# Kernel tuning notes

Measured on AMD Instinct MI355X. Metric: run time of the kernel, lower is better.

Reference implementation:

```python
import jax, jax.numpy as jnp
import numpy as np


def _structure_constants():
    # Octonion multiplication table: e_i * e_j = sum_k C[i,j,k] e_k.
    # e0 is the real unit; imaginary triples follow the standard Fano-plane
    # convention (Baez): e_a e_b = e_c for the cyclic triples below.
    C = np.zeros((8, 8, 8), dtype=np.float32)
    C[0, 0, 0] = 1.0
    for i in range(1, 8):
        C[0, i, i] = 1.0   # 1 * e_i = e_i
        C[i, 0, i] = 1.0   # e_i * 1 = e_i
        C[i, i, 0] = -1.0  # e_i * e_i = -1
    triples = [(1, 2, 3), (1, 4, 5), (1, 7, 6), (2, 4, 6), (2, 5, 7), (3, 4, 7), (3, 6, 5)]
    for (a, b, c) in triples:
        for (p, q, r) in ((a, b, c), (b, c, a), (c, a, b)):
            C[p, q, r] = 1.0
            C[q, p, r] = -1.0
    return C


_C = _structure_constants()

IN_FEATURES = 64
OUT_FEATURES = 64
BATCH = (16, 4096)


def setup_inputs() -> dict:
    key = jax.random.key(0)
    kx, kw, kb = jax.random.split(key, 3)
    x = jax.random.normal(kx, (*BATCH, IN_FEATURES, 8), dtype=jnp.float32)
    # 8 octonion-component weight matrices, stacked: [8, out, in]
    scale = 1.0 / np.sqrt(IN_FEATURES * 8)
    W = jax.random.normal(kw, (8, OUT_FEATURES, IN_FEATURES), dtype=jnp.float32) * scale
    b = jax.random.normal(kb, (OUT_FEATURES, 8), dtype=jnp.float32) * 0.01
    return {"x": x, "W": W, "b": b}


def reference(x, W, b):
    # out[..., o, k] = sum_{i,j,f} C[i,j,k] * W[i,o,f] * x[..., f, j] + b[o, k]
    # Fold the sparse structure constants into one block weight, then a single
    # contraction (the fused-GEMM formulation of the original 64-linear loop).
    C = jnp.asarray(_C, dtype=x.dtype)
    Wbig = jnp.einsum('iof,ijk->okfj', W, C)        # [out, 8, in, 8]
    out = jnp.einsum('...fj,okfj->...ok', x, Wbig)  # [..., out, 8]
    return out + b
```

## Files before the change

### kernel.cpp

```cpp
#include <hip/hip_runtime.h>
#include <hip/hip_bf16.h>

typedef __attribute__((ext_vector_type(8))) short short8;
typedef __attribute__((ext_vector_type(4))) float f32x4;
typedef __attribute__((address_space(1))) const unsigned int as1_u32;
typedef __attribute__((address_space(3))) unsigned int as3_u32;

#define BM 256
#define BN 256
#define BK 64
#define LDSTA 72
#define NKT 8
#define A_ELE (256 * LDSTA)
#define B_ELE (256 * 64)
#define LDS_BYTES ((2 * A_ELE + 2 * B_ELE) * 2)

static __device__ __forceinline__ unsigned short f2bf(float f) {
    union { __hip_bfloat16 h; unsigned short u; } cv;
    cv.h = __float2bfloat16(f);
    return cv.u;
}

__device__ __forceinline__ void gload16(const unsigned short* g, unsigned short* l) {
    __builtin_amdgcn_global_load_lds((as1_u32*)g, (as3_u32*)l, 16, 0, 0);
}

__global__ __launch_bounds__(256) void build_wbig(const float* __restrict__ W,
                                                  unsigned short* __restrict__ WbigS) {
    __shared__ float C[8][8][8];
    const int t = threadIdx.x;
    for (int i = t; i < 512; i += 256) ((float*)C)[i] = 0.0f;
    __syncthreads();
    if (t == 0) {
        C[0][0][0] = 1.0f;
        for (int i = 1; i < 8; ++i) { C[0][i][i] = 1.0f; C[i][0][i] = 1.0f; C[i][i][0] = -1.0f; }
        const int tr[7][3] = {{1,2,3},{1,4,5},{1,7,6},{2,4,6},{2,5,7},{3,4,7},{3,6,5}};
        for (int q = 0; q < 7; ++q) {
            const int a = tr[q][0], b = tr[q][1], c = tr[q][2];
            const int p[3][3] = {{a,b,c},{b,c,a},{c,a,b}};
            for (int u = 0; u < 3; ++u) {
                C[p[u][0]][p[u][1]][p[u][2]] = 1.0f;
                C[p[u][1]][p[u][0]][p[u][2]] = -1.0f;
            }
        }
    }
    __syncthreads();
    const int e = blockIdx.x * 256 + t;
    const int m = e >> 9, kk = e & 511;
    const int o = m >> 3, k = m & 7, f = kk >> 3, j = kk & 7;
    float s = 0.0f;
#pragma unroll
    for (int i = 0; i < 8; ++i) s += C[i][j][k] * W[i * 4096 + o * 64 + f];

    const int ntile = m >> 8, row = m & 255;
    const int kt = kk >> 6, c = kk & 63;
    const int g_st = (c >> 3) ^ (row & 7);
    WbigS[((((size_t)(ntile * 8 + kt) * 256 + row) * 8 + g_st) * 8) + (c & 7)] = f2bf(s);
}

__global__ __launch_bounds__(512, 2) void oct_gemm(const float* __restrict__ X,
                                                   const unsigned short* __restrict__ WbigS,
                                                   const float* __restrict__ Bias,
                                                   float* __restrict__ Out) {
    extern __shared__ unsigned short smem[];
    unsigned short* As[2] = { smem,             smem + A_ELE };
    unsigned short* Bs[2] = { smem + 2 * A_ELE, smem + 2 * A_ELE + B_ELE };

    const int bid   = blockIdx.x;
    const int xcd   = bid & 7;
    const int ix    = bid >> 3;
    const int mtile = xcd * 32 + (ix >> 1);
    const int ntile = ix & 1;
    const int rowBase = mtile * BM;
    const int colBase = ntile * BN;

    const int t    = threadIdx.x;
    const int lane = t & 63;
    const int w    = t >> 6;
    const int wr   = w >> 2;
    const int wc   = w & 3;
    const int l15  = lane & 15;
    const int l4   = lane >> 4;

    const int srow = t >> 3;
    const int scol = (t & 7) * 8;
    const float* Xrow = X + (size_t)(rowBase + srow) * 512 + scol;

    f32x4 va0[8], va1[8];

#define ISSUE_A(VA, KT) do { _Pragma("unroll") \
    for (int l = 0; l < 4; ++l) { \
        const float* src = Xrow + (size_t)(l * 64) * 512 + (KT) * BK; \
        VA[2*l]   = *reinterpret_cast<const f32x4*>(src); \
        VA[2*l+1] = *reinterpret_cast<const f32x4*>(src + 4); \
    } } while (0)

#define WRITE_A(VA, BUF) do { _Pragma("unroll") \
    for (int l = 0; l < 4; ++l) { \
        short8 p; \
        p[0]=(short)f2bf(VA[2*l][0]);   p[1]=(short)f2bf(VA[2*l][1]); \
        p[2]=(short)f2bf(VA[2*l][2]);   p[3]=(short)f2bf(VA[2*l][3]); \
        p[4]=(short)f2bf(VA[2*l+1][0]); p[5]=(short)f2bf(VA[2*l+1][1]); \
        p[6]=(short)f2bf(VA[2*l+1][2]); p[7]=(short)f2bf(VA[2*l+1][3]); \
        *reinterpret_cast<short8*>(&As[BUF][(l*64 + srow) * LDSTA + scol]) = p; \
    } } while (0)

#define GLOAD_B(BUF, KT) do { _Pragma("unroll") \
    for (int j = 0; j < 4; ++j) \
        gload16(WbigS + ((size_t)(ntile * 8 + (KT)) << 14) + (((w * 4 + j) * 64 + lane) << 3), \
                Bs[BUF] + ((w * 4 + j) << 9)); \
    } while (0)

    f32x4 acc[8][4];
#pragma unroll
    for (int ni = 0; ni < 4; ++ni) {
        const float bv = Bias[colBase + wc * 64 + ni * 16 + l15];
#pragma unroll
        for (int mi = 0; mi < 8; ++mi) acc[mi][ni] = (f32x4){bv, bv, bv, bv};
    }

    ISSUE_A(va0, 0);
    GLOAD_B(0, 0);
    ISSUE_A(va1, 1);
    WRITE_A(va0, 0);
    asm volatile("s_waitcnt vmcnt(8) lgkmcnt(0)" ::: "memory");
    __builtin_amdgcn_s_barrier();

#pragma unroll
    for (int kt = 0; kt < NKT; ++kt) {
        if (kt + 1 < NKT) GLOAD_B((kt + 1) & 1, kt + 1);
        if (kt + 2 < NKT) { if ((kt & 1) == 0) ISSUE_A(va0, kt + 2); else ISSUE_A(va1, kt + 2); }
        __builtin_amdgcn_sched_barrier(0);

#pragma unroll
        for (int kk = 0; kk < 2; ++kk) {
            short8 b[4];
#pragma unroll
            for (int ni = 0; ni < 4; ++ni) {
                const int row = wc * 64 + ni * 16 + l15;
                const int gs  = ((kk * 4 + l4) ^ (l15 & 7)) * 8;
                b[ni] = *reinterpret_cast<const short8*>(&Bs[kt & 1][row * 64 + gs]);
            }
            __builtin_amdgcn_s_setprio(1);
#pragma unroll
            for (int mi = 0; mi < 8; ++mi) {
                const short8 a = *reinterpret_cast<const short8*>(
                    &As[kt & 1][(wr * 128 + mi * 16 + l15) * LDSTA + kk * 32 + l4 * 8]);
#pragma unroll
                for (int ni = 0; ni < 4; ++ni)
                    acc[mi][ni] = __builtin_amdgcn_mfma_f32_16x16x32_bf16(
                        a, b[ni], acc[mi][ni], 0, 0, 0);
            }
            __builtin_amdgcn_s_setprio(0);
        }
        __builtin_amdgcn_sched_barrier(0);

        if (kt + 1 < NKT) { if ((kt & 1) == 0) WRITE_A(va1, 1); else WRITE_A(va0, 0); }

        if (kt + 2 < NKT)
            asm volatile("s_waitcnt vmcnt(8) lgkmcnt(0)" ::: "memory");
        else if (kt + 1 < NKT)
            asm volatile("s_waitcnt vmcnt(0) lgkmcnt(0)" ::: "memory");
        else
            asm volatile("s_waitcnt lgkmcnt(0)" ::: "memory");
        __builtin_amdgcn_s_barrier();
    }

#pragma unroll
    for (int mi = 0; mi < 8; ++mi) {
        const int row0 = rowBase + wr * 128 + mi * 16 + l4 * 4;
#pragma unroll
        for (int ni = 0; ni < 4; ++ni) {
            const int col = colBase + wc * 64 + ni * 16 + l15;
#pragma unroll
            for (int r = 0; r < 4; ++r)
                Out[(size_t)(row0 + r) * 512 + col] = acc[mi][ni][r];
        }
    }
#undef ISSUE_A
#undef WRITE_A
#undef GLOAD_B
}

extern "C" void kernel_launch(void* const* d_in, const int* in_sizes, int n_in,
                              void* d_out, int out_size, void* d_ws, size_t ws_size,
                              hipStream_t stream) {
    const float* x = (const float*)d_in[0];
    const float* W = (const float*)d_in[1];
    const float* b = (const float*)d_in[2];
    float* out = (float*)d_out;
    unsigned short* WbigS = (unsigned short*)d_ws;

    static bool attr_done = false;
    if (!attr_done) {
        hipFuncSetAttribute((const void*)oct_gemm,
                            hipFuncAttributeMaxDynamicSharedMemorySize, LDS_BYTES);
        attr_done = true;
    }

    build_wbig<<<1024, 256, 0, stream>>>(W, WbigS);
    oct_gemm<<<512, 512, LDS_BYTES, stream>>>(x, WbigS, b, out);
}
```

Measured before the change: 65.00 us.

## Interleave global loads and LDS writes between MFMA phases with barrier-staged pipeline

Reworks the GEMM main loop so each K-tile is split into four MFMA phases separated by workgroup barriers. Global loads of the next A and B tiles and the bf16 conversion and LDS writes are interleaved between these phases, in the style of a ping-pong schedule. The B weight layout in the workspace changes to two 32-wide K halves with a new XOR swizzle. The A staging changes to 2 threads per row with a single-stage register prefetch. The change aims to hide load latency behind MFMA work, but it adds many barriers per iteration and shortens the prefetch distance for A.

```diff
diff --git a/kernel.cpp b/kernel.cpp
--- a/kernel.cpp
+++ b/kernel.cpp
@@ -9,10 +9,10 @@
 #define BM 256
 #define BN 256
 #define BK 64
+#define NKT 8
 #define LDSTA 72
-#define NKT 8
 #define A_ELE (256 * LDSTA)
-#define B_ELE (256 * 64)
+#define B_ELE (2 * 8192)
 #define LDS_BYTES ((2 * A_ELE + 2 * B_ELE) * 2)
 
 static __device__ __forceinline__ unsigned short f2bf(float f) {
@@ -21,7 +21,7 @@
     return cv.u;
 }
 
-__device__ __forceinline__ void gload16(const unsigned short* g, unsigned short* l) {
+__device__ __forceinline__ void gload16(const void* g, void* l) {
     __builtin_amdgcn_global_load_lds((as1_u32*)g, (as3_u32*)l, 16, 0, 0);
 }
 
@@ -52,10 +52,9 @@
 #pragma unroll
     for (int i = 0; i < 8; ++i) s += C[i][j][k] * W[i * 4096 + o * 64 + f];
 
-    const int ntile = m >> 8, row = m & 255;
-    const int kt = kk >> 6, c = kk & 63;
-    const int g_st = (c >> 3) ^ (row & 7);
-    WbigS[((((size_t)(ntile * 8 + kt) * 256 + row) * 8 + g_st) * 8) + (c & 7)] = f2bf(s);
+    const int nt = m >> 8, c = m & 255;
+    const int H = kk >> 5, g = (kk >> 3) & 3, e8 = kk & 7;
+    WbigS[((size_t)(nt * 16 + H) << 13) + 32 * c + 8 * (g ^ ((c >> 1) & 3)) + e8] = f2bf(s);
 }
 
 __global__ __launch_bounds__(512, 2) void oct_gemm(const float* __restrict__ X,
@@ -63,16 +62,16 @@
                                                    const float* __restrict__ Bias,
                                                    float* __restrict__ Out) {
     extern __shared__ unsigned short smem[];
-    unsigned short* As[2] = { smem,             smem + A_ELE };
-    unsigned short* Bs[2] = { smem + 2 * A_ELE, smem + 2 * A_ELE + B_ELE };
-
-    const int bid   = blockIdx.x;
-    const int xcd   = bid & 7;
-    const int ix    = bid >> 3;
+    unsigned short* As[2]  = { smem,             smem + A_ELE };
+    unsigned short* Bsm[2] = { smem + 2 * A_ELE, smem + 2 * A_ELE + B_ELE };
+
+    const int bid = blockIdx.x;
+    const int xcd = bid & 7;
+    const int ix  = bid >> 3;
     const int mtile = xcd * 32 + (ix >> 1);
-    const int ntile = ix & 1;
+    const int nt    = ix & 1;
     const int rowBase = mtile * BM;
-    const int colBase = ntile * BN;
+    const int colBase = nt * BN;
 
     const int t    = threadIdx.x;
     const int lane = t & 63;
@@ -82,34 +81,43 @@
     const int l15  = lane & 15;
     const int l4   = lane >> 4;
 
-    const int srow = t >> 3;
-    const int scol = (t & 7) * 8;
-    const float* Xrow = X + (size_t)(rowBase + srow) * 512 + scol;
-
-    f32x4 va0[8], va1[8];
-
-#define ISSUE_A(VA, KT) do { _Pragma("unroll") \
-    for (int l = 0; l < 4; ++l) { \
-        const float* src = Xrow + (size_t)(l * 64) * 512 + (KT) * BK; \
-        VA[2*l]   = *reinterpret_cast<const f32x4*>(src); \
-        VA[2*l+1] = *reinterpret_cast<const f32x4*>(src + 4); \
-    } } while (0)
-
-#define WRITE_A(VA, BUF) do { _Pragma("unroll") \
-    for (int l = 0; l < 4; ++l) { \
-        short8 p; \
-        p[0]=(short)f2bf(VA[2*l][0]);   p[1]=(short)f2bf(VA[2*l][1]); \
-        p[2]=(short)f2bf(VA[2*l][2]);   p[3]=(short)f2bf(VA[2*l][3]); \
-        p[4]=(short)f2bf(VA[2*l+1][0]); p[5]=(short)f2bf(VA[2*l+1][1]); \
-        p[6]=(short)f2bf(VA[2*l+1][2]); p[7]=(short)f2bf(VA[2*l+1][3]); \
-        *reinterpret_cast<short8*>(&As[BUF][(l*64 + srow) * LDSTA + scol]) = p; \
-    } } while (0)
-
-#define GLOAD_B(BUF, KT) do { _Pragma("unroll") \
-    for (int j = 0; j < 4; ++j) \
-        gload16(WbigS + ((size_t)(ntile * 8 + (KT)) << 14) + (((w * 4 + j) * 64 + lane) << 3), \
-                Bs[BUF] + ((w * 4 + j) << 9)); \
-    } while (0)
+    const int arow = t >> 1;
+    const int acol = (t & 1) * 16;
+    const float* Xp = X + (size_t)(rowBase + arow) * 512 + acol;
+
+    const unsigned short* Bsrc = WbigS + ((size_t)(nt * 16) << 13) + ((size_t)t << 3);
+
+    f32x4 va0[4], va1[4];
+
+#define ISSUE_A(VA, KT, H) do { _Pragma("unroll") \
+    for (int l = 0; l < 4; ++l) \
+        VA[l] = *reinterpret_cast<const f32x4*>(Xp + (KT) * BK + (H) * 32 + l * 4); \
+    } while (0)
+
+#define WRITE_A(VA, NB, H) do { \
+    short8 p0, p1; \
+    p0[0]=(short)f2bf(VA[0][0]); p0[1]=(short)f2bf(VA[0][1]); \
+    p0[2]=(short)f2bf(VA[0][2]); p0[3]=(short)f2bf(VA[0][3]); \
+    p0[4]=(short)f2bf(VA[1][0]); p0[5]=(short)f2bf(VA[1][1]); \
+    p0[6]=(short)f2bf(VA[1][2]); p0[7]=(short)f2bf(VA[1][3]); \
+    p1[0]=(short)f2bf(VA[2][0]); p1[1]=(short)f2bf(VA[2][1]); \
+    p1[2]=(short)f2bf(VA[2][2]); p1[3]=(short)f2bf(VA[2][3]); \
+    p1[4]=(short)f2bf(VA[3][0]); p1[5]=(short)f2bf(VA[3][1]); \
+    p1[6]=(short)f2bf(VA[3][2]); p1[7]=(short)f2bf(VA[3][3]); \
+    *reinterpret_cast<short8*>(&As[NB][arow * LDSTA + (H) * 32 + acol]) = p0; \
+    *reinterpret_cast<short8*>(&As[NB][arow * LDSTA + (H) * 32 + acol + 8]) = p1; \
+    } while (0)
+
+#define GLOAD_B(NB, KT) do { _Pragma("unroll") \
+    for (int h = 0; h < 2; ++h) \
+        _Pragma("unroll") \
+        for (int i = 0; i < 2; ++i) \
+            gload16(Bsrc + ((size_t)(2 * (KT) + h) << 13) + (i * 512 << 3), \
+                    Bsm[NB] + h * 8192 + i * 4096 + w * 512); \
+    } while (0)
+
+    const int aoff = (wr * 128 + l15) * LDSTA + l4 * 8;
+    const int boff = (wc * 64 + l15) * 32 + ((l4 ^ ((l15 >> 1) & 3)) << 3);
 
     f32x4 acc[8][4];
 #pragma unroll
@@ -119,51 +127,61 @@
         for (int mi = 0; mi < 8; ++mi) acc[mi][ni] = (f32x4){bv, bv, bv, bv};
     }
 
-    ISSUE_A(va0, 0);
+    ISSUE_A(va0, 0, 0); ISSUE_A(va1, 0, 1);
     GLOAD_B(0, 0);
-    ISSUE_A(va1, 1);
-    WRITE_A(va0, 0);
-    asm volatile("s_waitcnt vmcnt(8) lgkmcnt(0)" ::: "memory");
-    __builtin_amdgcn_s_barrier();
+    WRITE_A(va0, 0, 0); WRITE_A(va1, 0, 1);
+    __syncthreads();
+
+#define MFMA_PAIR(Q) do { \
+    __builtin_amdgcn_s_setprio(1); \
+    _Pragma("unroll") \
+    for (int m2 = 0; m2 < 2; ++m2) { \
+        const int mi = 2 * (Q) + m2; \
+        _Pragma("unroll") \
+        for (int kk = 0; kk < 2; ++kk) { \
+            const short8 a = *reinterpret_cast<const short8*>( \
+                &As[buf][aoff + mi * (16 * LDSTA) + kk * 32]); \
+            _Pragma("unroll") \
+            for (int ni = 0; ni < 4; ++ni) \
+                acc[mi][ni] = __builtin_amdgcn_mfma_f32_16x16x32_bf16( \
+                    a, bf[kk][ni], acc[mi][ni], 0, 0, 0); \
+        } \
+    } \
+    __builtin_amdgcn_s_setprio(0); \
+    } while (0)
 
 #pragma unroll
     for (int kt = 0; kt < NKT; ++kt) {
-        if (kt + 1 < NKT) GLOAD_B((kt + 1) & 1, kt + 1);
-        if (kt + 2 < NKT) { if ((kt & 1) == 0) ISSUE_A(va0, kt + 2); else ISSUE_A(va1, kt + 2); }
-        __builtin_amdgcn_sched_barrier(0);
-
-#pragma unroll
-        for (int kk = 0; kk < 2; ++kk) {
-            short8 b[4];
-#pragma unroll
-            for (int ni = 0; ni < 4; ++ni) {
-                const int row = wc * 64 + ni * 16 + l15;
-                const int gs  = ((kk * 4 + l4) ^ (l15 & 7)) * 8;
-                b[ni] = *reinterpret_cast<const short8*>(&Bs[kt & 1][row * 64 + gs]);
-            }
-            __builtin_amdgcn_s_setprio(1);
-#pragma unroll
-            for (int mi = 0; mi < 8; ++mi) {
-                const short8 a = *reinterpret_cast<const short8*>(
-                    &As[kt & 1][(wr * 128 + mi * 16 + l15) * LDSTA + kk * 32 + l4 * 8]);
-#pragma unroll
-                for (int ni = 0; ni < 4; ++ni)
-                    acc[mi][ni] = __builtin_amdgcn_mfma_f32_16x16x32_bf16(
-                        a, b[ni], acc[mi][ni], 0, 0, 0);
-            }
-            __builtin_amdgcn_s_setprio(0);
-        }
-        __builtin_amdgcn_sched_barrier(0);
-
-        if (kt + 1 < NKT) { if ((kt & 1) == 0) WRITE_A(va1, 1); else WRITE_A(va0, 0); }
-
-        if (kt + 2 < NKT)
-            asm volatile("s_waitcnt vmcnt(8) lgkmcnt(0)" ::: "memory");
-        else if (kt + 1 < NKT)
-            asm volatile("s_waitcnt vmcnt(0) lgkmcnt(0)" ::: "memory");
-        else
-            asm volatile("s_waitcnt lgkmcnt(0)" ::: "memory");
-        __builtin_amdgcn_s_barrier();
+        const int buf = kt & 1, nbuf = buf ^ 1;
+        const bool pre = (kt + 1 < NKT);
+
+        short8 bf[2][4];
+#pragma unroll
+        for (int kk = 0; kk < 2; ++kk)
+#pragma unroll
+            for (int ni = 0; ni < 4; ++ni)
+                bf[kk][ni] = *reinterpret_cast<const short8*>(
+                    &Bsm[buf][kk * 8192 + boff + ni * 512]);
+
+        if (pre) { GLOAD_B(nbuf, kt + 1); ISSUE_A(va0, kt + 1, 0); }
+        __builtin_amdgcn_s_barrier();
+        MFMA_PAIR(0);
+        __builtin_amdgcn_s_barrier();
+
+        if (pre) ISSUE_A(va1, kt + 1, 1);
+        __builtin_amdgcn_s_barrier();
+        MFMA_PAIR(1);
+        __builtin_amdgcn_s_barrier();
+
+        if (pre) WRITE_A(va0, nbuf, 0);
+        __builtin_amdgcn_s_barrier();
+        MFMA_PAIR(2);
+        __builtin_amdgcn_s_barrier();
+
+        if (pre) WRITE_A(va1, nbuf, 1);
+        __builtin_amdgcn_s_barrier();
+        MFMA_PAIR(3);
+        __syncthreads();
     }
 
 #pragma unroll
@@ -180,6 +198,7 @@
 #undef ISSUE_A
 #undef WRITE_A
 #undef GLOAD_B
+#undef MFMA_PAIR
 }
 
 extern "C" void kernel_launch(void* const* d_in, const int* in_sizes, int n_in,
```

Result: slower. 77.68 us (+19.5%).
